# Performance work log

Hardware: AMD Instinct MI355X
Metric: run time of the kernel (lower is better)

Reference implementation:

```python
import jax, jax.numpy as jnp
import numpy as np

B, T, C = 2, 2048, 1024
NH, HD = 16, 64  # n_head, head_dim (qk == vo)


def setup_inputs() -> dict:
    key = jax.random.key(0)
    ks = jax.random.split(key, 5)
    scale = 1.0 / np.sqrt(C)
    return {
        "x": jax.random.normal(ks[0], (B, T, C), dtype=jnp.float32),
        "Wq": jax.random.normal(ks[1], (C, C), dtype=jnp.float32) * scale,
        "Wk": jax.random.normal(ks[2], (C, C), dtype=jnp.float32) * scale,
        "Wv": jax.random.normal(ks[3], (C, C), dtype=jnp.float32) * scale,
        "Wo": jax.random.normal(ks[4], (C, C), dtype=jnp.float32) * scale,
    }


def reference(x, Wq, Wk, Wv, Wo):
    # torch Linear: y = x @ W.T (weights stored [out, in])
    q = (x @ Wq.T).reshape(B, T, NH, HD).transpose(0, 2, 1, 3)  # [B,H,T,D]
    k = (x @ Wk.T).reshape(B, T, NH, HD).transpose(0, 2, 1, 3)
    v = (x @ Wv.T).reshape(B, T, NH, HD).transpose(0, 2, 1, 3)
    att = jnp.einsum("bhqd,bhkd->bhqk", q, k) * (1.0 / np.sqrt(HD))
    causal = jnp.tril(jnp.ones((T, T), dtype=bool))
    att = jnp.where(causal[None, None], att, -jnp.inf)
    att = jax.nn.softmax(att, axis=-1)
    y = jnp.einsum("bhqk,bhkd->bhqd", att, v)  # [B,H,T,D]
    y = y.transpose(0, 2, 1, 3).reshape(B, T, NH * HD)
    return y @ Wo.T  # dropout p=0 -> identity
```

## Files before the change

### kernel.cpp

```cpp
#include <hip/hip_runtime.h>
#include <hip/hip_bf16.h>
#include <cstdint>
#include <cstddef>
#include <cmath>

#define B_  2
#define T_  2048
#define C_  1024
#define NH_ 16
#define HD_ 64

typedef __bf16 bf16;
typedef bf16  bf16x8 __attribute__((ext_vector_type(8)));
typedef bf16  bf16x4 __attribute__((ext_vector_type(4)));
typedef float f32x4  __attribute__((ext_vector_type(4)));

#define MFMA16(a, b, c) __builtin_amdgcn_mfma_f32_16x16x32_bf16((a), (b), (c), 0, 0, 0)

__device__ __forceinline__ void gld_lds16(const bf16* g, bf16* lds_base_uniform) {
    __builtin_amdgcn_global_load_lds(
        (const __attribute__((address_space(1))) uint32_t*)g,
        (__attribute__((address_space(3))) uint32_t*)lds_base_uniform,
        16, 0, 0);
}

__global__ __launch_bounds__(256) void cast_all(const float* __restrict__ x,
                                                const float* __restrict__ Wq,
                                                const float* __restrict__ Wk,
                                                const float* __restrict__ Wv,
                                                const float* __restrict__ Wo,
                                                bf16* __restrict__ xb,
                                                bf16* __restrict__ Wqk,
                                                bf16* __restrict__ Wvb,
                                                bf16* __restrict__ Wob) {
    const int bid = blockIdx.x;
    if (bid < 4096) {
        const int i = bid * 256 + threadIdx.x;
        float4 v = ((const float4*)x)[i];
        ((bf16x4*)xb)[i] = bf16x4{ (bf16)v.x, (bf16)v.y, (bf16)v.z, (bf16)v.w };
    } else {
        const float C1 = 0.1803368801111f;
        const int i = (bid - 4096) * 256 + threadIdx.x;
        const int nw4 = C_ * C_ / 4;
        float4 q = ((const float4*)Wq)[i];
        float4 k = ((const float4*)Wk)[i];
        float4 v = ((const float4*)Wv)[i];
        float4 o = ((const float4*)Wo)[i];
        ((bf16x4*)Wqk)[i]       = bf16x4{ (bf16)(q.x * C1), (bf16)(q.y * C1),
                                          (bf16)(q.z * C1), (bf16)(q.w * C1) };
        ((bf16x4*)Wqk)[nw4 + i] = bf16x4{ (bf16)k.x, (bf16)k.y, (bf16)k.z, (bf16)k.w };
        ((bf16x4*)Wvb)[i]       = bf16x4{ (bf16)v.x, (bf16)v.y, (bf16)v.z, (bf16)v.w };
        ((bf16x4*)Wob)[i]       = bf16x4{ (bf16)o.x, (bf16)o.y, (bf16)o.z, (bf16)o.w };
    }
}

__device__ __forceinline__ void gemm_tile(bf16* As, bf16* Bs,
                                          const bf16* __restrict__ A,
                                          const bf16* __restrict__ W,
                                          bf16* __restrict__ Y,
                                          int N, int K, int m0, int n0) {
    const int tid  = threadIdx.x;
    const int lane = tid & 63;
    const int w    = tid >> 6;
    const int ml   = lane & 15;
    const int quad = lane >> 4;
    const int wm   = (w >> 1) * 64;
    const int wn   = (w & 1) * 64;
    const int sr   = lane >> 2;
    const int sc   = lane & 3;

    f32x4 acc[4][4] = {};

    for (int k0 = 0; k0 < K; k0 += 32) {
        __syncthreads();
#pragma unroll
        for (int ei = 0; ei < 2; ++ei) {
            const int e = w * 2 + ei;
            gld_lds16(A + (size_t)(m0 + e * 16 + sr) * K + k0 + sc * 8, &As[e * 512]);
            gld_lds16(W + (size_t)(n0 + e * 16 + sr) * K + k0 + sc * 8, &Bs[e * 512]);
        }
        __builtin_amdgcn_s_waitcnt(0);
        __syncthreads();

        bf16x8 af[4], bfr[4];
#pragma unroll
        for (int t = 0; t < 4; ++t) {
            af[t]  = *(const bf16x8*)&As[(wm + t * 16 + ml) * 32 + quad * 8];
            bfr[t] = *(const bf16x8*)&Bs[(wn + t * 16 + ml) * 32 + quad * 8];
        }
#pragma unroll
        for (int mt = 0; mt < 4; ++mt)
#pragma unroll
            for (int nt = 0; nt < 4; ++nt)
                acc[mt][nt] = MFMA16(af[mt], bfr[nt], acc[mt][nt]);
    }

#pragma unroll
    for (int mt = 0; mt < 4; ++mt)
#pragma unroll
        for (int nt = 0; nt < 4; ++nt)
#pragma unroll
            for (int r = 0; r < 4; ++r) {
                const int row = m0 + wm + mt * 16 + quad * 4 + r;
                const int col = n0 + wn + nt * 16 + ml;
                Y[(size_t)row * N + col] = (bf16)acc[mt][nt][r];
            }
}

__global__ __launch_bounds__(256) void proj_fused(const bf16* __restrict__ xb,
                                                  const bf16* __restrict__ Wqk,
                                                  const bf16* __restrict__ Wvb,
                                                  bf16* __restrict__ QKb,
                                                  bf16* __restrict__ VtT) {
    __shared__ __align__(16) bf16 As[128 * 32];
    __shared__ __align__(16) bf16 Bs[128 * 32];
    const int bid = blockIdx.x;
    if (bid < 512) {
        gemm_tile(As, Bs, xb, Wqk, QKb, 2048, 1024, (bid >> 4) * 128, (bid & 15) * 128);
    } else {
        const int b2 = bid - 512;
        gemm_tile(As, Bs, Wvb, xb, VtT, 4096, 1024, (b2 >> 5) * 128, (b2 & 31) * 128);
    }
}

__global__ __launch_bounds__(256) void gemm_wo(const bf16* __restrict__ A,
                                               const bf16* __restrict__ W,
                                               float* __restrict__ Y) {
    __shared__ __align__(16) bf16 As[64 * 32];
    __shared__ __align__(16) bf16 Bs[128 * 32];
    const int tid  = threadIdx.x;
    const int lane = tid & 63;
    const int w    = tid >> 6;
    const int ml   = lane & 15;
    const int quad = lane >> 4;
    const int wm   = (w >> 1) * 32;
    const int wn   = (w & 1) * 64;
    const int m0   = blockIdx.y * 64;
    const int n0   = blockIdx.x * 128;
    const int sr   = lane >> 2;
    const int sc   = lane & 3;

    f32x4 acc[2][4] = {};

    for (int k0 = 0; k0 < 1024; k0 += 32) {
        __syncthreads();
        gld_lds16(A + (size_t)(m0 + w * 16 + sr) * 1024 + k0 + sc * 8, &As[w * 512]);
#pragma unroll
        for (int ei = 0; ei < 2; ++ei) {
            const int e = w * 2 + ei;
            gld_lds16(W + (size_t)(n0 + e * 16 + sr) * 1024 + k0 + sc * 8, &Bs[e * 512]);
        }
        __builtin_amdgcn_s_waitcnt(0);
        __syncthreads();

        bf16x8 af[2], bfr[4];
#pragma unroll
        for (int t = 0; t < 2; ++t)
            af[t] = *(const bf16x8*)&As[(wm + t * 16 + ml) * 32 + quad * 8];
#pragma unroll
        for (int t = 0; t < 4; ++t)
            bfr[t] = *(const bf16x8*)&Bs[(wn + t * 16 + ml) * 32 + quad * 8];
#pragma unroll
        for (int mt = 0; mt < 2; ++mt)
#pragma unroll
            for (int nt = 0; nt < 4; ++nt)
                acc[mt][nt] = MFMA16(af[mt], bfr[nt], acc[mt][nt]);
    }

#pragma unroll
    for (int mt = 0; mt < 2; ++mt)
#pragma unroll
        for (int nt = 0; nt < 4; ++nt)
#pragma unroll
            for (int r = 0; r < 4; ++r) {
                const int row = m0 + wm + mt * 16 + quad * 4 + r;
                const int col = n0 + wn + nt * 16 + ml;
                Y[(size_t)row * 1024 + col] = acc[mt][nt][r];
            }
}

__global__ __launch_bounds__(256, 4) void attn_mfma(const bf16* __restrict__ QKb,
                                                    const bf16* __restrict__ VtT,
                                                    bf16* __restrict__ Pbuf,
                                                    float* __restrict__ Lbuf) {
    const int bid  = blockIdx.x;
    const int hb   = bid & 31;
    const int s    = 79 - (bid >> 5);
    int qt, chunk;
    if (s < 8)       { qt = s;                   chunk = 0; }
    else if (s < 24) { qt = 8  + ((s - 8) >> 1); chunk = (s - 8) & 1; }
    else if (s < 48) { qt = 16 + (s - 24) / 3;   chunk = (s - 24) % 3; }
    else             { qt = 24 + ((s - 48) >> 2); chunk = (s - 48) & 3; }
    const int h = hb >> 1, b = hb & 1;

    const int tid  = threadIdx.x;
    const int lane = tid & 63;
    const int w    = tid >> 6;
    const int ml   = lane & 15;
    const int quad = lane >> 4;

    __shared__ __align__(16) bf16 Ks[2][4096];
    __shared__ __align__(16) bf16 Vs[4096];
    __shared__ __align__(16) bf16 Ps[4][16 * 64];

    const bf16* Qbase = QKb + (size_t)b * T_ * 2048 + (size_t)h * HD_;
    const bf16* Kbase = Qbase + 1024;
    const bf16* Vbase = VtT + (size_t)h * HD_ * 4096 + (size_t)b * T_;

    const int qrow = qt * 64 + w * 16 + ml;
    bf16x8 qf[2];
#pragma unroll
    for (int ks = 0; ks < 2; ++ks)
        qf[ks] = *(const bf16x8*)(Qbase + (size_t)qrow * 2048 + ks * 32 + quad * 8);

    f32x4 o_acc[4] = {};
    f32x4 l_acc = {};
    bf16x8 onesf;
#pragma unroll
    for (int j = 0; j < 8; ++j) onesf[j] = (bf16)1.0f;

    const int sr = lane >> 2, sc = lane & 3;
    bf16* ps = &Ps[w][0];
    uint16_t* ps16 = (uint16_t*)ps;

    const int ktbase  = chunk * 8;
    const int nrounds = min(8, qt + 1 - ktbase);

    auto stageK = [&](int ktg, int buf) {
        const int k0 = ktg * 64;
#pragma unroll
        for (int ei = 0; ei < 2; ++ei) {
            const int e = w * 2 + ei;
            const int r = (e & 3) * 16 + sr;
            const int ch = (e >> 2) * 32 + sc * 8;
            gld_lds16(Kbase + (size_t)(k0 + r) * 2048 + ch, &Ks[buf][e * 512]);
        }
    };
    auto stageV = [&](int ktg) {
        const int k0 = ktg * 64;
#pragma unroll
        for (int ei = 0; ei < 2; ++ei) {
            const int e = w * 2 + ei;
            const int r = (e & 3) * 16 + sr;
            const int ch = (e >> 2) * 32 + sc * 8;
            gld_lds16(Vbase + (size_t)r * 4096 + k0 + ch, &Vs[e * 512]);
        }
    };

    auto phase1 = [&](int cur, int ktg) {
        const int k0 = ktg * 64;
#pragma unroll
        for (int nt = 0; nt < 4; ++nt) {
            f32x4 sacc = {};
#pragma unroll
            for (int ks = 0; ks < 2; ++ks) {
                bf16x8 kf = *(const bf16x8*)&Ks[cur][ks * 2048 + (nt * 16 + ml) * 32 + quad * 8];
                sacc = MFMA16(qf[ks], kf, sacc);
            }
            const int kg = k0 + nt * 16 + ml;
#pragma unroll
            for (int r = 0; r < 4; ++r) {
                float arg = sacc[r];
                if (ktg == qt) {
                    const int qg = qt * 64 + w * 16 + quad * 4 + r;
                    if (kg > qg) arg = -1e30f;
                }
                const float p = __builtin_amdgcn_exp2f(arg);
                const int row = quad * 4 + r;
                ps16[row * 64 + ((nt * 16 + ml) ^ ((row & 7) << 3))] =
                    (uint16_t)(__builtin_bit_cast(uint32_t, p) >> 16);
            }
        }
    };

    auto phase2 = [&]() {
#pragma unroll
        for (int ks = 0; ks < 2; ++ks) {
            bf16x8 pf = *(const bf16x8*)&ps[ml * 64 + ((((ks << 2) + quad) ^ (ml & 7)) << 3)];
            l_acc = MFMA16(pf, onesf, l_acc);
#pragma unroll
            for (int nt = 0; nt < 4; ++nt) {
                bf16x8 vf = *(const bf16x8*)&Vs[ks * 2048 + (nt * 16 + ml) * 32 + quad * 8];
                o_acc[nt] = MFMA16(pf, vf, o_acc[nt]);
            }
        }
    };

    stageK(ktbase, 0);

    for (int j = 0; j < nrounds; ++j) {
        const int cur = j & 1;
        const int ktg = ktbase + j;

        asm volatile("s_barrier" ::: "memory");
        stageV(ktg);
        if (j + 1 < nrounds) {
            stageK(ktg + 1, cur ^ 1);
            asm volatile("s_waitcnt vmcnt(4)" ::: "memory");
            asm volatile("s_barrier" ::: "memory");
            phase1(cur, ktg);
            asm volatile("s_waitcnt vmcnt(2)" ::: "memory");
            asm volatile("s_barrier" ::: "memory");
            phase2();
        } else {
            asm volatile("s_waitcnt vmcnt(2)" ::: "memory");
            asm volatile("s_barrier" ::: "memory");
            phase1(cur, ktg);
            asm volatile("s_waitcnt vmcnt(0)" ::: "memory");
            asm volatile("s_barrier" ::: "memory");
            phase2();
        }
    }

    const int slotIdx = hb * 80 + s;
    bf16* pb = Pbuf + (size_t)slotIdx * 4096;
#pragma unroll
    for (int r = 0; r < 4; ++r) {
        const int prow = w * 16 + quad * 4 + r;
#pragma unroll
        for (int nt = 0; nt < 4; ++nt)
            pb[prow * 64 + nt * 16 + ml] = (bf16)o_acc[nt][r];
        if (ml == 0)
            Lbuf[slotIdx * 64 + prow] = l_acc[r];
    }
}

__global__ __launch_bounds__(256) void attn_merge(const bf16* __restrict__ Pbuf,
                                                  const float* __restrict__ Lbuf,
                                                  bf16* __restrict__ Ab) {
    const int gid = blockIdx.x;
    const int qt  = gid >> 5;
    const int hb  = gid & 31;
    const int h = hb >> 1, b = hb & 1;
    int s0;
    if (qt < 8)       s0 = qt;
    else if (qt < 16) s0 = 8 + (qt - 8) * 2;
    else if (qt < 24) s0 = 24 + (qt - 16) * 3;
    else              s0 = 48 + (qt - 24) * 4;
    const int nch = (qt + 8) >> 3;

    const int tid = threadIdx.x;
    const int row = tid >> 2;
    const int cg  = (tid & 3) * 16;

    float acc[16] = {};
    float lsum = 0.f;
    for (int c = 0; c < nch; ++c) {
        const int slotIdx = hb * 80 + s0 + c;
        lsum += Lbuf[slotIdx * 64 + row];
        const bf16* pb = Pbuf + (size_t)slotIdx * 4096 + row * 64 + cg;
        bf16x8 v0 = *(const bf16x8*)pb;
        bf16x8 v1 = *(const bf16x8*)(pb + 8);
#pragma unroll
        for (int j = 0; j < 8; ++j) { acc[j] += (float)v0[j]; acc[8 + j] += (float)v1[j]; }
    }
    const float rcl = 1.0f / lsum;
    bf16x8 o0, o1;
#pragma unroll
    for (int j = 0; j < 8; ++j) { o0[j] = (bf16)(acc[j] * rcl); o1[j] = (bf16)(acc[8 + j] * rcl); }
    bf16* dst = Ab + (size_t)(b * T_ + qt * 64 + row) * 1024 + h * 64 + cg;
    *(bf16x8*)dst = o0;
    *(bf16x8*)(dst + 8) = o1;
}

extern "C" void kernel_launch(void* const* d_in, const int* in_sizes, int n_in,
                              void* d_out, int out_size, void* d_ws, size_t ws_size,
                              hipStream_t stream) {
    const float* x  = (const float*)d_in[0];
    const float* Wq = (const float*)d_in[1];
    const float* Wk = (const float*)d_in[2];
    const float* Wv = (const float*)d_in[3];
    const float* Wo = (const float*)d_in[4];
    float* out = (float*)d_out;

    const size_t n_x = (size_t)B_ * T_ * C_;
    const size_t n_w = (size_t)C_ * C_;

    bf16* xb   = (bf16*)d_ws;
    bf16* Wqk  = xb + n_x;
    bf16* Wvb  = Wqk + 2 * n_w;
    bf16* Wob  = Wvb + n_w;
    bf16* QKb  = Wob + n_w;
    bf16* VtT  = QKb + 2 * n_x;
    bf16* Ab   = VtT + n_x;
    bf16* Pbuf = Ab + n_x;
    float* Lbuf = (float*)(Pbuf + (size_t)2560 * 4096);

    cast_all<<<5120, 256, 0, stream>>>(x, Wq, Wk, Wv, Wo, xb, Wqk, Wvb, Wob);

    proj_fused<<<768, 256, 0, stream>>>(xb, Wqk, Wvb, QKb, VtT);

    attn_mfma<<<2560, 256, 0, stream>>>(QKb, VtT, Pbuf, Lbuf);
    attn_merge<<<1024, 256, 0, stream>>>(Pbuf, Lbuf, Ab);

    gemm_wo<<<dim3(1024 / 128, 4096 / 64), 256, 0, stream>>>(Ab, Wob, out);
}
```

Baseline: 182.8 us.

## Double-buffer V alongside K and prefetch both one tile ahead

The V tile is now double-buffered like K, and both are prefetched together for the next key tile while the current tile's QK and PV MFMAs run. Per-iteration barriers drop from three to one, and the V load latency that used to be exposed before phase2 is hidden. The cost is an extra 8 KB of LDS per block, which may reduce occupancy. Reusing the per-wave P buffer between phase1 and phase2 relies on intra-wave ordering only.

```diff
diff --git a/kernel.cpp b/kernel.cpp
--- a/kernel.cpp
+++ b/kernel.cpp
@@ -200,7 +200,7 @@
     const int quad = lane >> 4;
 
     __shared__ __align__(16) bf16 Ks[2][4096];
-    __shared__ __align__(16) bf16 Vs[4096];
+    __shared__ __align__(16) bf16 Vs[2][4096];
     __shared__ __align__(16) bf16 Ps[4][16 * 64];
 
     const bf16* Qbase = QKb + (size_t)b * T_ * 2048 + (size_t)h * HD_;
@@ -226,7 +226,7 @@
     const int ktbase  = chunk * 8;
     const int nrounds = min(8, qt + 1 - ktbase);
 
-    auto stageK = [&](int ktg, int buf) {
+    auto stageKV = [&](int ktg, int buf) {
         const int k0 = ktg * 64;
 #pragma unroll
         for (int ei = 0; ei < 2; ++ei) {
@@ -234,16 +234,7 @@
             const int r = (e & 3) * 16 + sr;
             const int ch = (e >> 2) * 32 + sc * 8;
             gld_lds16(Kbase + (size_t)(k0 + r) * 2048 + ch, &Ks[buf][e * 512]);
-        }
-    };
-    auto stageV = [&](int ktg) {
-        const int k0 = ktg * 64;
-#pragma unroll
-        for (int ei = 0; ei < 2; ++ei) {
-            const int e = w * 2 + ei;
-            const int r = (e & 3) * 16 + sr;
-            const int ch = (e >> 2) * 32 + sc * 8;
-            gld_lds16(Vbase + (size_t)r * 4096 + k0 + ch, &Vs[e * 512]);
+            gld_lds16(Vbase + (size_t)r * 4096 + k0 + ch, &Vs[buf][e * 512]);
         }
     };
 
@@ -273,42 +264,33 @@
         }
     };
 
-    auto phase2 = [&]() {
+    auto phase2 = [&](int cur) {
 #pragma unroll
         for (int ks = 0; ks < 2; ++ks) {
             bf16x8 pf = *(const bf16x8*)&ps[ml * 64 + ((((ks << 2) + quad) ^ (ml & 7)) << 3)];
             l_acc = MFMA16(pf, onesf, l_acc);
 #pragma unroll
             for (int nt = 0; nt < 4; ++nt) {
-                bf16x8 vf = *(const bf16x8*)&Vs[ks * 2048 + (nt * 16 + ml) * 32 + quad * 8];
+                bf16x8 vf = *(const bf16x8*)&Vs[cur][ks * 2048 + (nt * 16 + ml) * 32 + quad * 8];
                 o_acc[nt] = MFMA16(pf, vf, o_acc[nt]);
             }
         }
     };
 
-    stageK(ktbase, 0);
+    stageKV(ktbase, 0);
+    asm volatile("s_waitcnt vmcnt(0)" ::: "memory");
+    asm volatile("s_barrier" ::: "memory");
 
     for (int j = 0; j < nrounds; ++j) {
         const int cur = j & 1;
         const int ktg = ktbase + j;
 
-        asm volatile("s_barrier" ::: "memory");
-        stageV(ktg);
+        if (j + 1 < nrounds) stageKV(ktg + 1, cur ^ 1);
+        phase1(cur, ktg);
+        phase2(cur);
         if (j + 1 < nrounds) {
-            stageK(ktg + 1, cur ^ 1);
-            asm volatile("s_waitcnt vmcnt(4)" ::: "memory");
-            asm volatile("s_barrier" ::: "memory");
-            phase1(cur, ktg);
-            asm volatile("s_waitcnt vmcnt(2)" ::: "memory");
-            asm volatile("s_barrier" ::: "memory");
-            phase2();
-        } else {
-            asm volatile("s_waitcnt vmcnt(2)" ::: "memory");
-            asm volatile("s_barrier" ::: "memory");
-            phase1(cur, ktg);
             asm volatile("s_waitcnt vmcnt(0)" ::: "memory");
             asm volatile("s_barrier" ::: "memory");
-            phase2();
         }
     }
 
```

Result: no change. 185.9 us (+1.7%).
